# Kernel tuning notes

Measured on AMD Instinct MI355X. Metric: run time of the kernel, lower is better.

The kernel has to match this reference:

```python
import jax, jax.numpy as jnp
import numpy as np

N = 100000  # num nodes
E = 3200000  # num edges (before self-loops)


def setup_inputs() -> dict:
    key = jax.random.key(0)
    k1, k2, k3, k4 = jax.random.split(key, 4)
    x = jax.random.normal(k1, (N, 128), dtype=jnp.float32)
    edge_index = jax.random.randint(k2, (2, E), 0, N, dtype=jnp.int64)
    W1 = jax.random.normal(k3, (128, 64), dtype=jnp.float32) * (1.0 / np.sqrt(128))
    b1 = jnp.zeros((64,), dtype=jnp.float32)
    W2 = jax.random.normal(k4, (64, 1), dtype=jnp.float32) * (1.0 / np.sqrt(64))
    b2 = jnp.zeros((1,), dtype=jnp.float32)
    return {"x": x, "edge_index": edge_index, "W1": W1, "b1": b1, "W2": W2, "b2": b2}


def _gcn_norm(edge_index, num_nodes):
    # add self-loops, then symmetric normalization deg^-1/2[row]*deg^-1/2[col]
    loops = jnp.arange(num_nodes, dtype=edge_index.dtype)
    row = jnp.concatenate([edge_index[0], loops])  # destination
    col = jnp.concatenate([edge_index[1], loops])  # source
    deg = jax.ops.segment_sum(jnp.ones_like(row, dtype=jnp.float32), row,
                              num_segments=num_nodes)
    dinv = jnp.where(deg > 0, jax.lax.rsqrt(deg), 0.0)
    norm = dinv[row] * dinv[col]  # [E+N]
    return row, col, norm


def _gcn_conv(x, row, col, norm, W, b, num_nodes):
    h = x @ W                                   # transform before propagate
    msg = h[col] * norm[:, None]                # gather + scale  [E+N, out]
    out = jax.ops.segment_sum(msg, row, num_segments=num_nodes)  # scatter-add
    return out + b


def reference(x, edge_index, W1, b1, W2, b2):
    row, col, norm = _gcn_norm(edge_index, N)
    h = _gcn_conv(x, row, col, norm, W1, b1, N)
    h = jax.nn.relu(h)
    # dropout p=0.0 -> identity
    h = _gcn_conv(h, row, col, norm, W2, b2, N)
    return jax.nn.sigmoid(h)
```

## Files before the change

kernel.cpp:

```cpp
#include <hip/hip_runtime.h>
#include <hip/hip_bf16.h>
#if __has_include(<hip/hip_fp8.h>)
#include <hip/hip_fp8.h>
#endif
#include <math.h>

#define BKT_SHIFT 8
#define BKT_W     256
#define NBP       512
#define CHUNK     8192
#define CAPR      9216
#define CAPC      11264

__device__ __forceinline__ float fp8_to_f32(int v) {
#if __has_builtin(__builtin_amdgcn_cvt_f32_fp8)
  return __builtin_amdgcn_cvt_f32_fp8(v, 0);
#else
  __hip_fp8_e4m3 t; t.__x = (unsigned char)v; return (float)t;
#endif
}

__device__ __forceinline__ unsigned f32x4_to_fp8x4(float a, float b, float c, float d) {
#if __has_builtin(__builtin_amdgcn_cvt_pk_fp8_f32)
  int w = __builtin_amdgcn_cvt_pk_fp8_f32(a, b, 0, false);
  w = __builtin_amdgcn_cvt_pk_fp8_f32(c, d, w, true);
  return (unsigned)w;
#else
  __hip_fp8_e4m3 t0(a), t1(b), t2(c), t3(d);
  return (unsigned)t0.__x | ((unsigned)t1.__x << 8) |
         ((unsigned)t2.__x << 16) | ((unsigned)t3.__x << 24);
#endif
}

__global__ void init_k(const unsigned* __restrict__ e, int* __restrict__ flag,
                       int* __restrict__ bcur, int nb) {
  int t = blockIdx.x * blockDim.x + threadIdx.x;
  if (t == 0) {
    int z = (e[1] == 0u) + (e[3] == 0u) + (e[5] == 0u) + (e[7] == 0u);
    *flag = (z == 4) ? 1 : 0;
  }
  if (t < nb) bcur[t] = t * CAPR;
}

__global__ __launch_bounds__(512) void bin_k(const void* __restrict__ ei, int* __restrict__ bcur,
                                             unsigned* __restrict__ recs, const int* __restrict__ flag,
                                             int E, int NB) {
  __shared__ unsigned srec[CHUNK];
  __shared__ int h[NBP], scex[NBP], cur[NBP], gb[NBP], s[NBP];
  int t = threadIdx.x;
  h[t] = 0;
  __syncthreads();
  bool f64 = (*flag) != 0;
  int start = blockIdx.x * CHUNK;
  int cntE = min(CHUNK, E - start);
  int r[16], c[16];
#pragma unroll
  for (int j = 0; j < 16; ++j) {
    int i = t + j * 512;
    int e = start + min(i, cntE - 1);
    if (f64) {
      r[j] = (int)((const long long*)ei)[e];
      c[j] = (int)((const long long*)ei)[(long long)E + e];
    } else {
      r[j] = ((const int*)ei)[e];
      c[j] = ((const int*)ei)[E + e];
    }
    if (i < cntE) atomicAdd(&h[r[j] >> BKT_SHIFT], 1);
  }
  __syncthreads();
  int v = h[t];
  s[t] = v;
  __syncthreads();
  for (int d = 1; d < NBP; d <<= 1) {
    int a = (t >= d) ? s[t - d] : 0;
    __syncthreads();
    s[t] += a;
    __syncthreads();
  }
  scex[t] = s[t] - v;
  cur[t] = s[t] - v;
  __syncthreads();
  if (t < NB && v) gb[t] = atomicAdd(&bcur[t], v);
#pragma unroll
  for (int j = 0; j < 16; ++j) {
    int i = t + j * 512;
    if (i < cntE) {
      int b = r[j] >> BKT_SHIFT;
      int slot = atomicAdd(&cur[b], 1);
      srec[slot] = ((unsigned)(r[j] & (BKT_W - 1)) << 17) | (unsigned)c[j];
    }
  }
  __syncthreads();
  for (int i = t; i < cntE; i += 512) {
    int lo = 0, hi = NB - 1;
    while (lo < hi) { int mid = (lo + hi + 1) >> 1; if (scex[mid] <= i) lo = mid; else hi = mid - 1; }
    recs[gb[lo] + (i - scex[lo])] = srec[i];
  }
}

__global__ __launch_bounds__(256) void csr_k(const unsigned* __restrict__ recs,
                                             const int* __restrict__ bcur,
                                             int* __restrict__ csr, int* __restrict__ offs,
                                             int* __restrict__ degs, float* __restrict__ dinv, int N) {
  __shared__ unsigned colbuf[CAPC];
  __shared__ int cnt[BKT_W], scx[BKT_W], cur[BKT_W], tmp[BKT_W];
  __shared__ int wtot;
  int t = threadIdx.x;
  int b = blockIdx.x;
  int rbase = b * CAPR;
  int size = min(bcur[b] - rbase, CAPR);
  int cbase = b * CAPC;
  int nb0 = b << BKT_SHIFT;
  int nNodes = min(BKT_W, N - nb0);
  cnt[t] = 0;
  __syncthreads();
  for (int i = t; i < size; i += 256) atomicAdd(&cnt[recs[rbase + i] >> 17], 1);
  __syncthreads();
  int myc = cnt[t];
  int seg = (myc + 7) & ~7;
  tmp[t] = seg;
  __syncthreads();
  for (int d = 1; d < BKT_W; d <<= 1) {
    int a = (t >= d) ? tmp[t - d] : 0;
    __syncthreads();
    tmp[t] += a;
    __syncthreads();
  }
  scx[t] = tmp[t] - seg;
  cur[t] = tmp[t] - seg;
  if (t == BKT_W - 1) wtot = tmp[t];
  __syncthreads();
  for (int i = t; i < size; i += 256) {
    unsigned rec = recs[rbase + i];
    int lr = rec >> 17;
    int slot = atomicAdd(&cur[lr], 1);
    colbuf[slot] = rec & 0x1FFFFu;
  }
  for (int i = scx[t] + myc; i < scx[t] + seg; ++i) colbuf[i] = (unsigned)N;
  __syncthreads();
  int wt = wtot;
  for (int i = t; i < wt; i += 256) csr[cbase + i] = colbuf[i];
  if (t < nNodes) {
    offs[nb0 + t] = cbase + scx[t];
    degs[nb0 + t] = myc;
    dinv[nb0 + t] = rsqrtf((float)(myc + 1));
  }
}

__global__ __launch_bounds__(256) void gemm_k(const float* __restrict__ x,
                                              const float* __restrict__ W1,
                                              const float* __restrict__ dinv,
                                              unsigned char* __restrict__ q8, int n) {
  __shared__ float4 xs[64 * 32];
  __shared__ float4 ws[64 * 16];
  int t = threadIdx.x;
  int row0 = blockIdx.x * 64;
  const float4* xg = (const float4*)x;
  const float4* wg = (const float4*)W1;
#pragma unroll
  for (int i = 0; i < 8; ++i) {
    int flat = t + i * 256;
    int r = flat >> 5, c = flat & 31;
    int gr = min(row0 + r, n - 1);
    xs[r * 32 + (c ^ (r & 31))] = xg[(size_t)gr * 32 + c];
  }
  int c4g = t & 15;
  int r4g = t >> 4;
  float acc[4][4];
#pragma unroll
  for (int j = 0; j < 4; ++j)
#pragma unroll
    for (int cc = 0; cc < 4; ++cc) acc[j][cc] = 0.f;
#pragma unroll
  for (int h = 0; h < 2; ++h) {
    if (h) __syncthreads();
#pragma unroll
    for (int i = 0; i < 4; ++i) {
      int flat = t + i * 256;
      ws[flat] = wg[(h * 64 + (flat >> 4)) * 16 + (flat & 15)];
    }
    __syncthreads();
#pragma unroll 2
    for (int k4 = 0; k4 < 16; ++k4) {
      float4 xv[4], wv[4];
#pragma unroll
      for (int j = 0; j < 4; ++j) {
        int r = r4g * 4 + j;
        xv[j] = xs[r * 32 + ((h * 16 + k4) ^ (r & 31))];
      }
#pragma unroll
      for (int kk = 0; kk < 4; ++kk) wv[kk] = ws[(k4 * 4 + kk) * 16 + c4g];
#pragma unroll
      for (int j = 0; j < 4; ++j) {
        acc[j][0] = fmaf(xv[j].x, wv[0].x, acc[j][0]);
        acc[j][1] = fmaf(xv[j].x, wv[0].y, acc[j][1]);
        acc[j][2] = fmaf(xv[j].x, wv[0].z, acc[j][2]);
        acc[j][3] = fmaf(xv[j].x, wv[0].w, acc[j][3]);
        acc[j][0] = fmaf(xv[j].y, wv[1].x, acc[j][0]);
        acc[j][1] = fmaf(xv[j].y, wv[1].y, acc[j][1]);
        acc[j][2] = fmaf(xv[j].y, wv[1].z, acc[j][2]);
        acc[j][3] = fmaf(xv[j].y, wv[1].w, acc[j][3]);
        acc[j][0] = fmaf(xv[j].z, wv[2].x, acc[j][0]);
        acc[j][1] = fmaf(xv[j].z, wv[2].y, acc[j][1]);
        acc[j][2] = fmaf(xv[j].z, wv[2].z, acc[j][2]);
        acc[j][3] = fmaf(xv[j].z, wv[2].w, acc[j][3]);
        acc[j][0] = fmaf(xv[j].w, wv[3].x, acc[j][0]);
        acc[j][1] = fmaf(xv[j].w, wv[3].y, acc[j][1]);
        acc[j][2] = fmaf(xv[j].w, wv[3].z, acc[j][2]);
        acc[j][3] = fmaf(xv[j].w, wv[3].w, acc[j][3]);
      }
    }
  }
#pragma unroll
  for (int j = 0; j < 4; ++j) {
    int r = row0 + r4g * 4 + j;
    if (r < n) {
      float di = dinv[r];
      unsigned w4 = f32x4_to_fp8x4(di * acc[j][0], di * acc[j][1],
                                   di * acc[j][2], di * acc[j][3]);
      ((unsigned*)q8)[(size_t)r * 16 + c4g] = w4;
    } else if (r == n) {
      ((unsigned*)q8)[(size_t)r * 16 + c4g] = 0u;
    }
  }
}

__global__ __launch_bounds__(256) void agg1_k(const unsigned char* __restrict__ q8,
                                              const int* __restrict__ offs,
                                              const int* __restrict__ degs,
                                              const int* __restrict__ csr,
                                              const float* __restrict__ dinv,
                                              const float* __restrict__ b1,
                                              const float* __restrict__ W2,
                                              float* __restrict__ p, int n) {
  int lane = threadIdx.x & 63;
  int wave = blockIdx.x * 4 + (threadIdx.x >> 6);
  int nw = gridDim.x * 4;
  float b1v = b1[lane];
  float w2v = W2[lane];
  for (int node = wave; node < n; node += nw) {
    int ns = __builtin_amdgcn_readfirstlane(node);
    int o0 = offs[ns];
    int dg = degs[ns];
    int dgp = (dg + 7) & ~7;
    float acc = 0.f;
    for (int b0 = 0; b0 < dgp; b0 += 64) {
      int rem = dgp - b0;
      int mm = rem < 64 ? rem : 64;
      int idx = n;
      if (lane < mm) idx = csr[o0 + b0 + lane];
      for (int e = 0; e < mm; e += 8) {
        int v[8];
#pragma unroll
        for (int k = 0; k < 8; ++k) {
          int c = __builtin_amdgcn_readlane(idx, e + k);
          v[k] = q8[((size_t)(unsigned)c << 6) + lane];
        }
#pragma unroll
        for (int k = 0; k < 8; ++k) acc += fp8_to_f32(v[k]);
      }
    }
    float selfv = fp8_to_f32((int)q8[((size_t)(unsigned)ns << 6) + lane]);
    float di = dinv[ns];
    float h = fmaf(di, acc + selfv, b1v);
    float tt = fmaxf(h, 0.f) * w2v;
    tt += __shfl_xor(tt, 1);  tt += __shfl_xor(tt, 2);  tt += __shfl_xor(tt, 4);
    tt += __shfl_xor(tt, 8);  tt += __shfl_xor(tt, 16); tt += __shfl_xor(tt, 32);
    if (lane == 0) p[ns] = di * tt;
  }
}

__global__ __launch_bounds__(256) void agg2_k(const float* __restrict__ p,
                                              const int* __restrict__ offs,
                                              const int* __restrict__ degs,
                                              const int* __restrict__ csr,
                                              const float* __restrict__ dinv,
                                              const float* __restrict__ b2,
                                              float* __restrict__ out, int n) {
  int lane = threadIdx.x & 63;
  int node = blockIdx.x * 4 + (threadIdx.x >> 6);
  if (node >= n) return;
  int o0 = offs[node];
  int dg = degs[node];
  float s = 0.f;
  for (int e = lane; e < dg; e += 64) s += p[csr[o0 + e]];
  s += __shfl_xor(s, 1); s += __shfl_xor(s, 2); s += __shfl_xor(s, 4);
  s += __shfl_xor(s, 8); s += __shfl_xor(s, 16); s += __shfl_xor(s, 32);
  if (lane == 0) {
    float z = fmaf(dinv[node], s + p[node], b2[0]);
    out[node] = 1.f / (1.f + expf(-z));
  }
}

extern "C" void kernel_launch(void* const* d_in, const int* in_sizes, int n_in,
                              void* d_out, int out_size, void* d_ws, size_t ws_size,
                              hipStream_t stream) {
  const float* x  = (const float*)d_in[0];
  const void*  ei = d_in[1];
  const float* W1 = (const float*)d_in[2];
  const float* b1 = (const float*)d_in[3];
  const float* W2 = (const float*)d_in[4];
  const float* b2 = (const float*)d_in[5];
  float* out = (float*)d_out;
  const int N = in_sizes[0] / 128;
  const int E = in_sizes[1] / 2;
  const int NB = (N + BKT_W - 1) >> BKT_SHIFT;
  const int nchunks = (E + CHUNK - 1) / CHUNK;
  (void)n_in; (void)out_size; (void)ws_size;

  char* base = (char*)d_ws;
  size_t off = 0;
  auto alloc = [&](size_t bytes) -> void* {
    void* ptr = base + off;
    off += (bytes + 1023) & ~(size_t)1023;
    return ptr;
  };
  int*   flag = (int*)alloc(64);
  int*   bcur = (int*)alloc((size_t)NBP * 4);
  int*   offs = (int*)alloc((size_t)N * 4);
  int*   degs = (int*)alloc((size_t)N * 4);
  float* dinv = (float*)alloc((size_t)N * 4);
  unsigned* recs = (unsigned*)alloc((size_t)NB * CAPR * 4);
  int*   csr  = (int*)alloc((size_t)NB * CAPC * 4);
  unsigned char* q8 = (unsigned char*)alloc(((size_t)N + 1) * 64);
  float* p    = (float*)alloc((size_t)N * 4);

  init_k<<<1, 512, 0, stream>>>((const unsigned*)ei, flag, bcur, NBP);
  bin_k<<<nchunks, 512, 0, stream>>>(ei, bcur, recs, flag, E, NB);
  csr_k<<<NB, 256, 0, stream>>>(recs, bcur, csr, offs, degs, dinv, N);
  gemm_k<<<(N + 64) / 64, 256, 0, stream>>>(x, W1, dinv, q8, N);
  agg1_k<<<2048, 256, 0, stream>>>(q8, offs, degs, csr, dinv, b1, W2, p, N);
  agg2_k<<<(N + 3) / 4, 256, 0, stream>>>(p, offs, degs, csr, dinv, b2, out, N);
}
```

Before: 166.9 us.

## Vectorize fp8 gather in agg1: 8 edges per wave with 8-byte loads

The first-layer aggregation kernel now gives each group of 8 lanes one neighbor's row, with each lane loading 8 fp8 values at once. A wave therefore handles 8 edges in parallel instead of one edge per 64 single-byte loads, and partial sums are combined with cross-group shuffles. To make this work, CSR segment padding rises from multiples of 8 to multiples of 32, which enlarges the per-bucket shared column buffer. The aim is fewer and wider memory transactions and less readlane serialization, at the cost of extra padding entries and more shared memory per block.

```diff
diff --git a/kernel.cpp b/kernel.cpp
--- a/kernel.cpp
+++ b/kernel.cpp
@@ -10,13 +10,14 @@
 #define NBP       512
 #define CHUNK     8192
 #define CAPR      9216
-#define CAPC      11264
-
-__device__ __forceinline__ float fp8_to_f32(int v) {
+#define CAPC      17408
+
+template <int SEL>
+__device__ __forceinline__ float fp8b(unsigned v) {
 #if __has_builtin(__builtin_amdgcn_cvt_f32_fp8)
-  return __builtin_amdgcn_cvt_f32_fp8(v, 0);
+  return __builtin_amdgcn_cvt_f32_fp8((int)v, SEL);
 #else
-  __hip_fp8_e4m3 t; t.__x = (unsigned char)v; return (float)t;
+  __hip_fp8_e4m3 t; t.__x = (unsigned char)(v >> (8 * SEL)); return (float)t;
 #endif
 }
 
@@ -117,7 +118,7 @@
   for (int i = t; i < size; i += 256) atomicAdd(&cnt[recs[rbase + i] >> 17], 1);
   __syncthreads();
   int myc = cnt[t];
-  int seg = (myc + 7) & ~7;
+  int seg = (myc + 31) & ~31;
   tmp[t] = seg;
   __syncthreads();
   for (int d = 1; d < BKT_W; d <<= 1) {
@@ -234,38 +235,69 @@
                                               const float* __restrict__ W2,
                                               float* __restrict__ p, int n) {
   int lane = threadIdx.x & 63;
+  int g = lane >> 3;
+  int l = lane & 7;
   int wave = blockIdx.x * 4 + (threadIdx.x >> 6);
   int nw = gridDim.x * 4;
-  float b1v = b1[lane];
-  float w2v = W2[lane];
+  float4 ba = ((const float4*)b1)[l * 2], bb = ((const float4*)b1)[l * 2 + 1];
+  float4 wa = ((const float4*)W2)[l * 2], wb = ((const float4*)W2)[l * 2 + 1];
+  float b1v[8] = {ba.x, ba.y, ba.z, ba.w, bb.x, bb.y, bb.z, bb.w};
+  float w2v[8] = {wa.x, wa.y, wa.z, wa.w, wb.x, wb.y, wb.z, wb.w};
+  int loff = l << 3;
   for (int node = wave; node < n; node += nw) {
     int ns = __builtin_amdgcn_readfirstlane(node);
     int o0 = offs[ns];
     int dg = degs[ns];
-    int dgp = (dg + 7) & ~7;
-    float acc = 0.f;
-    for (int b0 = 0; b0 < dgp; b0 += 64) {
-      int rem = dgp - b0;
-      int mm = rem < 64 ? rem : 64;
-      int idx = n;
-      if (lane < mm) idx = csr[o0 + b0 + lane];
-      for (int e = 0; e < mm; e += 8) {
-        int v[8];
-#pragma unroll
-        for (int k = 0; k < 8; ++k) {
-          int c = __builtin_amdgcn_readlane(idx, e + k);
-          v[k] = q8[((size_t)(unsigned)c << 6) + lane];
-        }
-#pragma unroll
-        for (int k = 0; k < 8; ++k) acc += fp8_to_f32(v[k]);
-      }
-    }
-    float selfv = fp8_to_f32((int)q8[((size_t)(unsigned)ns << 6) + lane]);
+    int dgp = (dg + 31) & ~31;
+    float acc[8] = {0.f, 0.f, 0.f, 0.f, 0.f, 0.f, 0.f, 0.f};
+    for (int eb = 0; eb < dgp; eb += 32) {
+      int base = o0 + eb + g;
+      int c0 = csr[base];
+      int c1 = csr[base + 8];
+      int c2 = csr[base + 16];
+      int c3 = csr[base + 24];
+      uint2 v0 = *(const uint2*)(q8 + (((size_t)(unsigned)c0) << 6) + loff);
+      uint2 v1 = *(const uint2*)(q8 + (((size_t)(unsigned)c1) << 6) + loff);
+      uint2 v2 = *(const uint2*)(q8 + (((size_t)(unsigned)c2) << 6) + loff);
+      uint2 v3 = *(const uint2*)(q8 + (((size_t)(unsigned)c3) << 6) + loff);
+      acc[0] += fp8b<0>(v0.x); acc[1] += fp8b<1>(v0.x);
+      acc[2] += fp8b<2>(v0.x); acc[3] += fp8b<3>(v0.x);
+      acc[4] += fp8b<0>(v0.y); acc[5] += fp8b<1>(v0.y);
+      acc[6] += fp8b<2>(v0.y); acc[7] += fp8b<3>(v0.y);
+      acc[0] += fp8b<0>(v1.x); acc[1] += fp8b<1>(v1.x);
+      acc[2] += fp8b<2>(v1.x); acc[3] += fp8b<3>(v1.x);
+      acc[4] += fp8b<0>(v1.y); acc[5] += fp8b<1>(v1.y);
+      acc[6] += fp8b<2>(v1.y); acc[7] += fp8b<3>(v1.y);
+      acc[0] += fp8b<0>(v2.x); acc[1] += fp8b<1>(v2.x);
+      acc[2] += fp8b<2>(v2.x); acc[3] += fp8b<3>(v2.x);
+      acc[4] += fp8b<0>(v2.y); acc[5] += fp8b<1>(v2.y);
+      acc[6] += fp8b<2>(v2.y); acc[7] += fp8b<3>(v2.y);
+      acc[0] += fp8b<0>(v3.x); acc[1] += fp8b<1>(v3.x);
+      acc[2] += fp8b<2>(v3.x); acc[3] += fp8b<3>(v3.x);
+      acc[4] += fp8b<0>(v3.y); acc[5] += fp8b<1>(v3.y);
+      acc[6] += fp8b<2>(v3.y); acc[7] += fp8b<3>(v3.y);
+    }
+#pragma unroll
+    for (int j = 0; j < 8; ++j) {
+      acc[j] += __shfl_xor(acc[j], 8);
+      acc[j] += __shfl_xor(acc[j], 16);
+      acc[j] += __shfl_xor(acc[j], 32);
+    }
+    uint2 sv = *(const uint2*)(q8 + (((size_t)(unsigned)ns) << 6) + loff);
     float di = dinv[ns];
-    float h = fmaf(di, acc + selfv, b1v);
-    float tt = fmaxf(h, 0.f) * w2v;
-    tt += __shfl_xor(tt, 1);  tt += __shfl_xor(tt, 2);  tt += __shfl_xor(tt, 4);
-    tt += __shfl_xor(tt, 8);  tt += __shfl_xor(tt, 16); tt += __shfl_xor(tt, 32);
+    float tt = 0.f;
+    {
+      float h0;
+      h0 = fmaf(di, acc[0] + fp8b<0>(sv.x), b1v[0]); tt += fmaxf(h0, 0.f) * w2v[0];
+      h0 = fmaf(di, acc[1] + fp8b<1>(sv.x), b1v[1]); tt += fmaxf(h0, 0.f) * w2v[1];
+      h0 = fmaf(di, acc[2] + fp8b<2>(sv.x), b1v[2]); tt += fmaxf(h0, 0.f) * w2v[2];
+      h0 = fmaf(di, acc[3] + fp8b<3>(sv.x), b1v[3]); tt += fmaxf(h0, 0.f) * w2v[3];
+      h0 = fmaf(di, acc[4] + fp8b<0>(sv.y), b1v[4]); tt += fmaxf(h0, 0.f) * w2v[4];
+      h0 = fmaf(di, acc[5] + fp8b<1>(sv.y), b1v[5]); tt += fmaxf(h0, 0.f) * w2v[5];
+      h0 = fmaf(di, acc[6] + fp8b<2>(sv.y), b1v[6]); tt += fmaxf(h0, 0.f) * w2v[6];
+      h0 = fmaf(di, acc[7] + fp8b<3>(sv.y), b1v[7]); tt += fmaxf(h0, 0.f) * w2v[7];
+    }
+    tt += __shfl_xor(tt, 1); tt += __shfl_xor(tt, 2); tt += __shfl_xor(tt, 4);
     if (lane == 0) p[ns] = di * tt;
   }
 }
```

Measured after the change: 173.9 us. +4.2%, slower.

## Split layer-1 aggregation by source-column halves to keep gathered features cache-resident

Applied to the files above, without the earlier changes.

The CSR build now partitions each node's neighbor list into two segments by source index (below/above SPLIT), each padded to 8. The first aggregation becomes two passes, each touching only half of the fp8 feature table so the working set is more likely to fit in cache. The first pass writes bf16 partial sums that the second pass reads back. Index loads are made nontemporal. agg2 now reads padding entries that point to a zeroed p[N] sentinel. This adds an extra kernel launch, a partial-sum buffer round trip, bf16 rounding of the partials, and more padding.

```diff
diff --git a/kernel.cpp b/kernel.cpp
--- a/kernel.cpp
+++ b/kernel.cpp
@@ -10,13 +10,15 @@
 #define NBP       512
 #define CHUNK     8192
 #define CAPR      9216
-#define CAPC      11264
-
-__device__ __forceinline__ float fp8_to_f32(int v) {
+#define CAPC      12800
+#define SPLIT     50688
+
+template <int SEL>
+__device__ __forceinline__ float fp8b(unsigned v) {
 #if __has_builtin(__builtin_amdgcn_cvt_f32_fp8)
-  return __builtin_amdgcn_cvt_f32_fp8(v, 0);
+  return __builtin_amdgcn_cvt_f32_fp8((int)v, SEL);
 #else
-  __hip_fp8_e4m3 t; t.__x = (unsigned char)v; return (float)t;
+  __hip_fp8_e4m3 t; t.__x = (unsigned char)(v >> (8 * SEL)); return (float)t;
 #endif
 }
 
@@ -33,11 +35,12 @@
 }
 
 __global__ void init_k(const unsigned* __restrict__ e, int* __restrict__ flag,
-                       int* __restrict__ bcur, int nb) {
+                       int* __restrict__ bcur, float* __restrict__ p, int N, int nb) {
   int t = blockIdx.x * blockDim.x + threadIdx.x;
   if (t == 0) {
     int z = (e[1] == 0u) + (e[3] == 0u) + (e[5] == 0u) + (e[7] == 0u);
     *flag = (z == 4) ? 1 : 0;
+    p[N] = 0.f;
   }
   if (t < nb) bcur[t] = t * CAPR;
 }
@@ -101,9 +104,11 @@
 __global__ __launch_bounds__(256) void csr_k(const unsigned* __restrict__ recs,
                                              const int* __restrict__ bcur,
                                              int* __restrict__ csr, int* __restrict__ offs,
-                                             int* __restrict__ degs, float* __restrict__ dinv, int N) {
+                                             int* __restrict__ lenA, int* __restrict__ lenT,
+                                             float* __restrict__ dinv, int N) {
   __shared__ unsigned colbuf[CAPC];
-  __shared__ int cnt[BKT_W], scx[BKT_W], cur[BKT_W], tmp[BKT_W];
+  __shared__ int cnt0[BKT_W], cnt1[BKT_W], scxA[BKT_W], scxB[BKT_W];
+  __shared__ int curA[BKT_W], curB[BKT_W], tmp[BKT_W];
   __shared__ int wtot;
   int t = threadIdx.x;
   int b = blockIdx.x;
@@ -112,38 +117,47 @@
   int cbase = b * CAPC;
   int nb0 = b << BKT_SHIFT;
   int nNodes = min(BKT_W, N - nb0);
-  cnt[t] = 0;
-  __syncthreads();
-  for (int i = t; i < size; i += 256) atomicAdd(&cnt[recs[rbase + i] >> 17], 1);
-  __syncthreads();
-  int myc = cnt[t];
-  int seg = (myc + 7) & ~7;
-  tmp[t] = seg;
-  __syncthreads();
-  for (int d = 1; d < BKT_W; d <<= 1) {
-    int a = (t >= d) ? tmp[t - d] : 0;
-    __syncthreads();
-    tmp[t] += a;
-    __syncthreads();
-  }
-  scx[t] = tmp[t] - seg;
-  cur[t] = tmp[t] - seg;
-  if (t == BKT_W - 1) wtot = tmp[t];
+  cnt0[t] = 0; cnt1[t] = 0;
   __syncthreads();
   for (int i = t; i < size; i += 256) {
     unsigned rec = recs[rbase + i];
     int lr = rec >> 17;
-    int slot = atomicAdd(&cur[lr], 1);
-    colbuf[slot] = rec & 0x1FFFFu;
-  }
-  for (int i = scx[t] + myc; i < scx[t] + seg; ++i) colbuf[i] = (unsigned)N;
+    atomicAdd(((rec & 0x1FFFFu) < SPLIT) ? &cnt0[lr] : &cnt1[lr], 1);
+  }
+  __syncthreads();
+  int c0 = cnt0[t], c1 = cnt1[t];
+  int p0 = (c0 + 7) & ~7, p1 = (c1 + 7) & ~7;
+  int seg = p0 + p1;
+  tmp[t] = seg;
+  __syncthreads();
+  for (int d = 1; d < BKT_W; d <<= 1) {
+    int a = (t >= d) ? tmp[t - d] : 0;
+    __syncthreads();
+    tmp[t] += a;
+    __syncthreads();
+  }
+  int nbase = tmp[t] - seg;
+  scxA[t] = nbase;      curA[t] = nbase;
+  scxB[t] = nbase + p0; curB[t] = nbase + p0;
+  if (t == BKT_W - 1) wtot = tmp[t];
+  __syncthreads();
+  for (int i = t; i < size; i += 256) {
+    unsigned rec = recs[rbase + i];
+    int lr = rec >> 17;
+    unsigned col = rec & 0x1FFFFu;
+    int slot = atomicAdd((col < SPLIT) ? &curA[lr] : &curB[lr], 1);
+    colbuf[slot] = col;
+  }
+  for (int i = scxA[t] + c0; i < scxA[t] + p0; ++i) colbuf[i] = (unsigned)N;
+  for (int i = scxB[t] + c1; i < scxB[t] + p1; ++i) colbuf[i] = (unsigned)N;
   __syncthreads();
   int wt = wtot;
   for (int i = t; i < wt; i += 256) csr[cbase + i] = colbuf[i];
   if (t < nNodes) {
-    offs[nb0 + t] = cbase + scx[t];
-    degs[nb0 + t] = myc;
-    dinv[nb0 + t] = rsqrtf((float)(myc + 1));
+    offs[nb0 + t] = cbase + scxA[t];
+    lenA[nb0 + t] = p0;
+    lenT[nb0 + t] = seg;
+    dinv[nb0 + t] = rsqrtf((float)(c0 + c1 + 1));
   }
 }
 
@@ -225,14 +239,51 @@
   }
 }
 
-__global__ __launch_bounds__(256) void agg1_k(const unsigned char* __restrict__ q8,
-                                              const int* __restrict__ offs,
-                                              const int* __restrict__ degs,
-                                              const int* __restrict__ csr,
-                                              const float* __restrict__ dinv,
-                                              const float* __restrict__ b1,
-                                              const float* __restrict__ W2,
-                                              float* __restrict__ p, int n) {
+__global__ __launch_bounds__(256) void agg1a_k(const unsigned char* __restrict__ q8,
+                                               const int* __restrict__ offs,
+                                               const int* __restrict__ lenA,
+                                               const int* __restrict__ csr,
+                                               unsigned short* __restrict__ part, int n) {
+  int lane = threadIdx.x & 63;
+  int wave = blockIdx.x * 4 + (threadIdx.x >> 6);
+  int nw = gridDim.x * 4;
+  for (int node = wave; node < n; node += nw) {
+    int ns = __builtin_amdgcn_readfirstlane(node);
+    int o0 = offs[ns];
+    int dgp = lenA[ns];
+    float acc = 0.f;
+    for (int b0 = 0; b0 < dgp; b0 += 64) {
+      int rem = dgp - b0;
+      int mm = rem < 64 ? rem : 64;
+      int idx = n;
+      if (lane < mm) idx = __builtin_nontemporal_load(csr + o0 + b0 + lane);
+      for (int e = 0; e < mm; e += 8) {
+        int v[8];
+#pragma unroll
+        for (int k = 0; k < 8; ++k) {
+          int c = __builtin_amdgcn_readlane(idx, e + k);
+          v[k] = q8[((size_t)(unsigned)c << 6) + lane];
+        }
+#pragma unroll
+        for (int k = 0; k < 8; ++k) acc += fp8b<0>((unsigned)v[k]);
+      }
+    }
+    __hip_bfloat16 hb = __float2bfloat16(acc);
+    __builtin_nontemporal_store(*reinterpret_cast<unsigned short*>(&hb),
+                                part + ((size_t)ns << 6) + lane);
+  }
+}
+
+__global__ __launch_bounds__(256) void agg1b_k(const unsigned char* __restrict__ q8,
+                                               const int* __restrict__ offs,
+                                               const int* __restrict__ lenA,
+                                               const int* __restrict__ lenT,
+                                               const int* __restrict__ csr,
+                                               const unsigned short* __restrict__ part,
+                                               const float* __restrict__ dinv,
+                                               const float* __restrict__ b1,
+                                               const float* __restrict__ W2,
+                                               float* __restrict__ p, int n) {
   int lane = threadIdx.x & 63;
   int wave = blockIdx.x * 4 + (threadIdx.x >> 6);
   int nw = gridDim.x * 4;
@@ -240,15 +291,15 @@
   float w2v = W2[lane];
   for (int node = wave; node < n; node += nw) {
     int ns = __builtin_amdgcn_readfirstlane(node);
-    int o0 = offs[ns];
-    int dg = degs[ns];
-    int dgp = (dg + 7) & ~7;
+    int la = lenA[ns];
+    int o0 = offs[ns] + la;
+    int dgp = lenT[ns] - la;
     float acc = 0.f;
     for (int b0 = 0; b0 < dgp; b0 += 64) {
       int rem = dgp - b0;
       int mm = rem < 64 ? rem : 64;
       int idx = n;
-      if (lane < mm) idx = csr[o0 + b0 + lane];
+      if (lane < mm) idx = __builtin_nontemporal_load(csr + o0 + b0 + lane);
       for (int e = 0; e < mm; e += 8) {
         int v[8];
 #pragma unroll
@@ -257,12 +308,14 @@
           v[k] = q8[((size_t)(unsigned)c << 6) + lane];
         }
 #pragma unroll
-        for (int k = 0; k < 8; ++k) acc += fp8_to_f32(v[k]);
+        for (int k = 0; k < 8; ++k) acc += fp8b<0>((unsigned)v[k]);
       }
     }
-    float selfv = fp8_to_f32((int)q8[((size_t)(unsigned)ns << 6) + lane]);
+    unsigned pa = part[((size_t)ns << 6) + lane];
+    acc += __uint_as_float(pa << 16);
+    acc += fp8b<0>((unsigned)q8[((size_t)(unsigned)ns << 6) + lane]);
     float di = dinv[ns];
-    float h = fmaf(di, acc + selfv, b1v);
+    float h = fmaf(di, acc, b1v);
     float tt = fmaxf(h, 0.f) * w2v;
     tt += __shfl_xor(tt, 1);  tt += __shfl_xor(tt, 2);  tt += __shfl_xor(tt, 4);
     tt += __shfl_xor(tt, 8);  tt += __shfl_xor(tt, 16); tt += __shfl_xor(tt, 32);
@@ -272,7 +325,7 @@
 
 __global__ __launch_bounds__(256) void agg2_k(const float* __restrict__ p,
                                               const int* __restrict__ offs,
-                                              const int* __restrict__ degs,
+                                              const int* __restrict__ lenT,
                                               const int* __restrict__ csr,
                                               const float* __restrict__ dinv,
                                               const float* __restrict__ b2,
@@ -281,9 +334,12 @@
   int node = blockIdx.x * 4 + (threadIdx.x >> 6);
   if (node >= n) return;
   int o0 = offs[node];
-  int dg = degs[node];
+  int dg = lenT[node];
   float s = 0.f;
-  for (int e = lane; e < dg; e += 64) s += p[csr[o0 + e]];
+  for (int e = lane; e < dg; e += 64) {
+    int c = __builtin_nontemporal_load(csr + o0 + e);
+    s += p[c];
+  }
   s += __shfl_xor(s, 1); s += __shfl_xor(s, 2); s += __shfl_xor(s, 4);
   s += __shfl_xor(s, 8); s += __shfl_xor(s, 16); s += __shfl_xor(s, 32);
   if (lane == 0) {
@@ -318,17 +374,20 @@
   int*   flag = (int*)alloc(64);
   int*   bcur = (int*)alloc((size_t)NBP * 4);
   int*   offs = (int*)alloc((size_t)N * 4);
-  int*   degs = (int*)alloc((size_t)N * 4);
+  int*   lenA = (int*)alloc((size_t)N * 4);
+  int*   lenT = (int*)alloc((size_t)N * 4);
   float* dinv = (float*)alloc((size_t)N * 4);
   unsigned* recs = (unsigned*)alloc((size_t)NB * CAPR * 4);
   int*   csr  = (int*)alloc((size_t)NB * CAPC * 4);
   unsigned char* q8 = (unsigned char*)alloc(((size_t)N + 1) * 64);
-  float* p    = (float*)alloc((size_t)N * 4);
-
-  init_k<<<1, 512, 0, stream>>>((const unsigned*)ei, flag, bcur, NBP);
+  unsigned short* part = (unsigned short*)alloc((size_t)N * 64 * 2);
+  float* p    = (float*)alloc(((size_t)N + 1) * 4);
+
+  init_k<<<1, 512, 0, stream>>>((const unsigned*)ei, flag, bcur, p, N, NBP);
   bin_k<<<nchunks, 512, 0, stream>>>(ei, bcur, recs, flag, E, NB);
-  csr_k<<<NB, 256, 0, stream>>>(recs, bcur, csr, offs, degs, dinv, N);
+  csr_k<<<NB, 256, 0, stream>>>(recs, bcur, csr, offs, lenA, lenT, dinv, N);
   gemm_k<<<(N + 64) / 64, 256, 0, stream>>>(x, W1, dinv, q8, N);
-  agg1_k<<<2048, 256, 0, stream>>>(q8, offs, degs, csr, dinv, b1, W2, p, N);
-  agg2_k<<<(N + 3) / 4, 256, 0, stream>>>(p, offs, degs, csr, dinv, b2, out, N);
-}
+  agg1a_k<<<2048, 256, 0, stream>>>(q8, offs, lenA, csr, part, N);
+  agg1b_k<<<2048, 256, 0, stream>>>(q8, offs, lenA, lenT, csr, part, dinv, b1, W2, p, N);
+  agg2_k<<<(N + 3) / 4, 256, 0, stream>>>(p, offs, lenT, csr, dinv, b2, out, N);
+}
```

Result: slower. 196.6 us (+17.8%).
